# Optimization experiments

Hardware: AMD Instinct MI355X
Metric: run time of the kernel (lower is better)

The kernel has to match this reference:

```python
import jax, jax.numpy as jnp
import numpy as np

D_ENC, D_PRED, D_JOINT, VOCAB = 512, 512, 640, 1024


def setup_inputs() -> dict:
    key = jax.random.key(0)
    k1, k2, k3, k4, k5, k6 = jax.random.split(key, 6)
    B, T, U1 = 8, 256, 64
    enc_out = jax.random.normal(k1, (B, T, D_ENC), dtype=jnp.float32)
    pred_out = jax.random.normal(k2, (B, U1, D_PRED), dtype=jnp.float32)
    # Linear weights, torch convention [out, in]; kaiming-uniform-ish scale
    W_enc = jax.random.normal(k3, (D_JOINT, D_ENC), dtype=jnp.float32) / np.sqrt(D_ENC)
    W_pred = jax.random.normal(k4, (D_JOINT, D_PRED), dtype=jnp.float32) / np.sqrt(D_PRED)
    W_out = jax.random.normal(k5, (VOCAB, D_JOINT), dtype=jnp.float32) / np.sqrt(D_JOINT)
    b_out = jax.random.normal(k6, (VOCAB,), dtype=jnp.float32) * 0.01
    return {"enc_out": enc_out, "pred_out": pred_out, "W_enc": W_enc,
            "W_pred": W_pred, "W_out": W_out, "b_out": b_out}


def reference(enc_out, pred_out, W_enc, W_pred, W_out, b_out):
    # f: [B, T, d_joint], g: [B, U+1, d_joint]
    f = jnp.einsum("btd,jd->btj", enc_out, W_enc)
    g = jnp.einsum("bud,jd->buj", pred_out, W_pred)
    # broadcast add -> [B, T, U+1, d_joint], tanh, project to vocab
    combined = jnp.tanh(f[:, :, None, :] + g[:, None, :, :])
    logits = jnp.einsum("btuj,vj->btuv", combined, W_out) + b_out
    return logits
```

## Files before the change

### kernel.cpp

```cpp
#include <hip/hip_runtime.h>


typedef _Float16 f16x8 __attribute__((ext_vector_type(8)));
typedef float    f32x4 __attribute__((ext_vector_type(4)));

__device__ __forceinline__ float fast_tanh(float x) {
    float e = __builtin_amdgcn_exp2f(x * 2.88539008177792681472f);
    return 1.0f - 2.0f * __builtin_amdgcn_rcpf(e + 1.0f);
}

__device__ __forceinline__ void gll16(const void* g, void* l) {
    __builtin_amdgcn_global_load_lds(
        (const __attribute__((address_space(1))) void*)g,
        (__attribute__((address_space(3))) void*)l, 16, 0, 0);
}

__global__ __launch_bounds__(256) void fg_kernel(
    const float* __restrict__ enc, const float* __restrict__ pred,
    const float* __restrict__ Wenc, const float* __restrict__ Wpred,
    float* __restrict__ fg)
{
    __shared__ float As[64][36];
    __shared__ float WsT[32][68];

    const int bid = blockIdx.x;
    const int mt = bid / 10;
    const int nt = bid % 10;
    const int m0 = mt * 64;
    const int n0 = nt * 64;

    const float* Aptr;
    const float* Wptr;
    if (m0 < 2048) { Aptr = enc  + (size_t)m0 * 512;          Wptr = Wenc; }
    else           { Aptr = pred + (size_t)(m0 - 2048) * 512; Wptr = Wpred; }

    const int t  = threadIdx.x;
    const int ty = t >> 4;
    const int tx = t & 15;
    const int lr = t >> 2;
    const int lc = (t & 3) * 8;
    const int lane6 = t & 63;
    const int w8    = (t >> 6) * 8;

    float acc[4][4];
#pragma unroll
    for (int i = 0; i < 4; ++i)
#pragma unroll
        for (int j = 0; j < 4; ++j) acc[i][j] = 0.0f;

    for (int k0 = 0; k0 < 512; k0 += 32) {
        __syncthreads();
        {
            const float* sa = Aptr + (size_t)lr * 512 + k0 + lc;
            f32x4 a0 = *(const f32x4*)(sa);
            f32x4 a1 = *(const f32x4*)(sa + 4);
            *(f32x4*)&As[lr][lc]     = a0;
            *(f32x4*)&As[lr][lc + 4] = a1;
            const float* sw = Wptr + (size_t)(n0 + lane6) * 512 + k0 + w8;
            f32x4 w0 = *(const f32x4*)(sw);
            f32x4 w1 = *(const f32x4*)(sw + 4);
#pragma unroll
            for (int j = 0; j < 4; ++j) {
                WsT[w8 + j][lane6]     = w0[j];
                WsT[w8 + 4 + j][lane6] = w1[j];
            }
        }
        __syncthreads();
#pragma unroll
        for (int kk = 0; kk < 32; ++kk) {
            float av[4], bv[4];
#pragma unroll
            for (int i = 0; i < 4; ++i) av[i] = As[ty * 4 + i][kk];
#pragma unroll
            for (int j = 0; j < 4; ++j) bv[j] = WsT[kk][tx * 4 + j];
#pragma unroll
            for (int i = 0; i < 4; ++i)
#pragma unroll
                for (int j = 0; j < 4; ++j)
                    acc[i][j] = fmaf(av[i], bv[j], acc[i][j]);
        }
    }

#pragma unroll
    for (int i = 0; i < 4; ++i) {
        f32x4 v = { acc[i][0], acc[i][1], acc[i][2], acc[i][3] };
        *(f32x4*)&fg[(size_t)(m0 + ty * 4 + i) * 640 + n0 + tx * 4] = v;
    }
}

__global__ __launch_bounds__(256) void wconv_kernel(
    const float* __restrict__ W, _Float16* __restrict__ Wh)
{
    const int idx = (blockIdx.x * 256 + threadIdx.x) * 8;
    f32x4 a = *(const f32x4*)(W + idx);
    f32x4 b = *(const f32x4*)(W + idx + 4);
    f16x8 h;
#pragma unroll
    for (int j = 0; j < 4; ++j) { h[j] = (_Float16)a[j]; h[4 + j] = (_Float16)b[j]; }
    *(f16x8*)(Wh + idx) = h;
}

__global__ __launch_bounds__(256, 2) void joint_kernel(
    const float* __restrict__ fg, const _Float16* __restrict__ Wh,
    const float* __restrict__ bias, float* __restrict__ out)
{
    __shared__ _Float16 Ash0[64 * 40];
    __shared__ _Float16 Ash1[64 * 40];
    __shared__ _Float16 Bsh0[512 * 32];
    __shared__ _Float16 Bsh1[512 * 32];

    const int bid = blockIdx.x;
    const int pp  = bid >> 1;
    const int mt  = (pp & 7) * 256 + (pp >> 3);
    const int nt  = bid & 1;
    const int m0  = mt << 6;
    const int n0  = nt << 9;

    const int t    = threadIdx.x;
    const int lane = t & 63;
    const int wid  = t >> 6;
    const int wn   = wid;
    const int lr   = lane & 15;
    const int lk   = lane >> 4;

    const int r  = t >> 2;
    const int q  = t & 3;
    const int m  = m0 + r;
    const float* grow = fg + (size_t)(2048 + ((m >> 14) << 6) + (m & 63)) * 640;
    const float* frow = fg + (size_t)(m >> 6) * 640;

    int aoff[4];
#pragma unroll
    for (int mf = 0; mf < 4; ++mf)
        aoff[mf] = (mf * 16 + lr) * 40 + lk * 8;
    int boff[8];
#pragma unroll
    for (int nf = 0; nf < 8; ++nf) {
        const int brow = wn * 128 + nf * 16 + lr;
        const int slot = lk ^ (brow & 3) ^ ((brow >> 2) & 3);
        boff[nf] = brow * 32 + slot * 8;
    }
    const int awoff = r * 40 + q * 8;

    const _Float16* gsrc[8];
    int gdst[8];
#pragma unroll
    for (int i = 0; i < 8; ++i) {
        const int seg  = wid * 8 + i;
        const int row  = (seg << 4) + (lane >> 2);
        const int c    = (lane & 3) ^ (row & 3) ^ ((row >> 2) & 3);
        gsrc[i] = Wh + (size_t)(n0 + row) * 640 + c * 8;
        gdst[i] = seg << 9;
    }

    f32x4 acc[4][8];
#pragma unroll
    for (int i = 0; i < 4; ++i)
#pragma unroll
        for (int j = 0; j < 8; ++j) acc[i][j] = (f32x4){0.f, 0.f, 0.f, 0.f};

    {
#pragma unroll
        for (int i = 0; i < 8; ++i)
            gll16(gsrc[i], &Bsh0[gdst[i]]);
        f32x4 fv0 = *(const f32x4*)(frow + q * 8);
        f32x4 fv1 = *(const f32x4*)(frow + q * 8 + 4);
        f32x4 gv0 = *(const f32x4*)(grow + q * 8);
        f32x4 gv1 = *(const f32x4*)(grow + q * 8 + 4);
        f16x8 h;
#pragma unroll
        for (int j = 0; j < 4; ++j) {
            h[j]     = (_Float16)fast_tanh(fv0[j] + gv0[j]);
            h[4 + j] = (_Float16)fast_tanh(fv1[j] + gv1[j]);
        }
        *(f16x8*)&Ash0[awoff] = h;
        __syncthreads();
    }

#define JITER_FULL(K0, CA, CB, NA, NB)                                         \
    {                                                                          \
        const int kn_ = (K0) + 32;                                             \
        _Pragma("unroll")                                                      \
        for (int i = 0; i < 8; ++i)                                            \
            gll16(gsrc[i] + kn_, &NB[gdst[i]]);                                \
        f32x4 fv0_ = *(const f32x4*)(frow + kn_ + q * 8);                      \
        f32x4 fv1_ = *(const f32x4*)(frow + kn_ + q * 8 + 4);                  \
        f32x4 gv0_ = *(const f32x4*)(grow + kn_ + q * 8);                      \
        f32x4 gv1_ = *(const f32x4*)(grow + kn_ + q * 8 + 4);                  \
        f16x8 af[4], bf[8];                                                    \
        _Pragma("unroll")                                                      \
        for (int mf = 0; mf < 4; ++mf)                                         \
            af[mf] = *(const f16x8*)&CA[aoff[mf]];                             \
        _Pragma("unroll")                                                      \
        for (int nf = 0; nf < 8; ++nf)                                         \
            bf[nf] = *(const f16x8*)&CB[boff[nf]];                             \
        f16x8 h_;                                                              \
        _Pragma("unroll")                                                      \
        for (int j = 0; j < 4; ++j) {                                          \
            h_[j]     = (_Float16)fast_tanh(fv0_[j] + gv0_[j]);                \
            h_[4 + j] = (_Float16)fast_tanh(fv1_[j] + gv1_[j]);                \
        }                                                                      \
        _Pragma("unroll")                                                      \
        for (int mf = 0; mf < 4; ++mf)                                         \
            _Pragma("unroll")                                                  \
            for (int nf = 0; nf < 8; ++nf)                                     \
                acc[mf][nf] = __builtin_amdgcn_mfma_f32_16x16x32_f16(          \
                    af[mf], bf[nf], acc[mf][nf], 0, 0, 0);                     \
        *(f16x8*)&NA[awoff] = h_;                                              \
        __syncthreads();                                                       \
    }

#define JITER_LAST(CA, CB)                                                     \
    {                                                                          \
        f16x8 af[4], bf[8];                                                    \
        _Pragma("unroll")                                                      \
        for (int mf = 0; mf < 4; ++mf)                                         \
            af[mf] = *(const f16x8*)&CA[aoff[mf]];                             \
        _Pragma("unroll")                                                      \
        for (int nf = 0; nf < 8; ++nf)                                         \
            bf[nf] = *(const f16x8*)&CB[boff[nf]];                             \
        _Pragma("unroll")                                                      \
        for (int mf = 0; mf < 4; ++mf)                                         \
            _Pragma("unroll")                                                  \
            for (int nf = 0; nf < 8; ++nf)                                     \
                acc[mf][nf] = __builtin_amdgcn_mfma_f32_16x16x32_f16(          \
                    af[mf], bf[nf], acc[mf][nf], 0, 0, 0);                     \
    }

    for (int kc = 0; kc < 18; kc += 2) {
        JITER_FULL(kc * 32,      Ash0, Bsh0, Ash1, Bsh1);
        JITER_FULL(kc * 32 + 32, Ash1, Bsh1, Ash0, Bsh0);
    }
    JITER_FULL(576, Ash0, Bsh0, Ash1, Bsh1);
    JITER_LAST(Ash1, Bsh1);

#undef JITER_FULL
#undef JITER_LAST

    float bv[8];
#pragma unroll
    for (int nf = 0; nf < 8; ++nf)
        bv[nf] = bias[n0 + wn * 128 + nf * 16 + lr];

#pragma unroll
    for (int mf = 0; mf < 4; ++mf) {
#pragma unroll
        for (int rr = 0; rr < 4; ++rr) {
            const int row = m0 + mf * 16 + lk * 4 + rr;
            float* orow = out + (size_t)row * 1024 + n0 + wn * 128;
#pragma unroll
            for (int nf = 0; nf < 8; ++nf)
                orow[nf * 16 + lr] = acc[mf][nf][rr] + bv[nf];
        }
    }
}

extern "C" void kernel_launch(void* const* d_in, const int* in_sizes, int n_in,
                              void* d_out, int out_size, void* d_ws, size_t ws_size,
                              hipStream_t stream) {
    const float* enc   = (const float*)d_in[0];
    const float* pred  = (const float*)d_in[1];
    const float* Wenc  = (const float*)d_in[2];
    const float* Wpred = (const float*)d_in[3];
    const float* Wout  = (const float*)d_in[4];
    const float* bout  = (const float*)d_in[5];

    float*     fg = (float*)d_ws;
    _Float16*  Wh = (_Float16*)((char*)d_ws + 2560 * 640 * 4);

    fg_kernel<<<400, 256, 0, stream>>>(enc, pred, Wenc, Wpred, fg);
    wconv_kernel<<<320, 256, 0, stream>>>(Wout, Wh);
    joint_kernel<<<4096, 256, 0, stream>>>(fg, Wh, bout, (float*)d_out);
}
```

Before: 355.9 us.

## Split joint GEMM k-step into four MFMA phases interleaved with loads and tanh

```diff
diff --git a/kernel.cpp b/kernel.cpp
--- a/kernel.cpp
+++ b/kernel.cpp
@@ -177,54 +177,80 @@
         __syncthreads();
     }
 
+    f16x8 af[4];
+    f16x8 hstage;
+
+#define JP_MFMA(P, BF0, BF1)                                                   \
+        __builtin_amdgcn_s_barrier();                                          \
+        __builtin_amdgcn_sched_barrier(0);                                     \
+        __builtin_amdgcn_s_setprio(1);                                         \
+        _Pragma("unroll")                                                      \
+        for (int mf = 0; mf < 4; ++mf) {                                       \
+            acc[mf][2 * (P)]     = __builtin_amdgcn_mfma_f32_16x16x32_f16(     \
+                af[mf], BF0, acc[mf][2 * (P)], 0, 0, 0);                       \
+            acc[mf][2 * (P) + 1] = __builtin_amdgcn_mfma_f32_16x16x32_f16(     \
+                af[mf], BF1, acc[mf][2 * (P) + 1], 0, 0, 0);                   \
+        }                                                                      \
+        __builtin_amdgcn_s_setprio(0);                                         \
+        __builtin_amdgcn_s_barrier();
+
 #define JITER_FULL(K0, CA, CB, NA, NB)                                         \
     {                                                                          \
         const int kn_ = (K0) + 32;                                             \
-        _Pragma("unroll")                                                      \
-        for (int i = 0; i < 8; ++i)                                            \
-            gll16(gsrc[i] + kn_, &NB[gdst[i]]);                                \
+                                \
+        f16x8 bf0, bf1;                                                        \
+        _Pragma("unroll")                                                      \
+        for (int mf = 0; mf < 4; ++mf)                                         \
+            af[mf] = *(const f16x8*)&CA[aoff[mf]];                             \
+        bf0 = *(const f16x8*)&CB[boff[0]];                                     \
+        bf1 = *(const f16x8*)&CB[boff[1]];                                     \
         f32x4 fv0_ = *(const f32x4*)(frow + kn_ + q * 8);                      \
         f32x4 fv1_ = *(const f32x4*)(frow + kn_ + q * 8 + 4);                  \
         f32x4 gv0_ = *(const f32x4*)(grow + kn_ + q * 8);                      \
         f32x4 gv1_ = *(const f32x4*)(grow + kn_ + q * 8 + 4);                  \
-        f16x8 af[4], bf[8];                                                    \
+        _Pragma("unroll")                                                      \
+        for (int i = 0; i < 4; ++i)                                            \
+            gll16(gsrc[i] + kn_, &NB[gdst[i]]);                                \
+        JP_MFMA(0, bf0, bf1)                                                   \
+                                \
+        bf0 = *(const f16x8*)&CB[boff[2]];                                     \
+        bf1 = *(const f16x8*)&CB[boff[3]];                                     \
+        _Pragma("unroll")                                                      \
+        for (int i = 4; i < 8; ++i)                                            \
+            gll16(gsrc[i] + kn_, &NB[gdst[i]]);                                \
+        JP_MFMA(1, bf0, bf1)                                                   \
+                                \
+        bf0 = *(const f16x8*)&CB[boff[4]];                                     \
+        bf1 = *(const f16x8*)&CB[boff[5]];                                     \
+        _Pragma("unroll")                                                      \
+        for (int j = 0; j < 4; ++j) {                                          \
+            hstage[j]     = (_Float16)fast_tanh(fv0_[j] + gv0_[j]);            \
+            hstage[4 + j] = (_Float16)fast_tanh(fv1_[j] + gv1_[j]);            \
+        }                                                                      \
+        JP_MFMA(2, bf0, bf1)                                                   \
+                                \
+        bf0 = *(const f16x8*)&CB[boff[6]];                                     \
+        bf1 = *(const f16x8*)&CB[boff[7]];                                     \
+        *(f16x8*)&NA[awoff] = hstage;                                          \
+        JP_MFMA(3, bf0, bf1)                                                   \
+        __syncthreads();                                                       \
+    }
+
+#define JITER_LAST(CA, CB)                                                     \
+    {                                                                          \
+        f16x8 bf[8];                                                           \
         _Pragma("unroll")                                                      \
         for (int mf = 0; mf < 4; ++mf)                                         \
             af[mf] = *(const f16x8*)&CA[aoff[mf]];                             \
         _Pragma("unroll")                                                      \
         for (int nf = 0; nf < 8; ++nf)                                         \
             bf[nf] = *(const f16x8*)&CB[boff[nf]];                             \
-        f16x8 h_;                                                              \
-        _Pragma("unroll")                                                      \
-        for (int j = 0; j < 4; ++j) {                                          \
-            h_[j]     = (_Float16)fast_tanh(fv0_[j] + gv0_[j]);                \
-            h_[4 + j] = (_Float16)fast_tanh(fv1_[j] + gv1_[j]);                \
-        }                                                                      \
         _Pragma("unroll")                                                      \
         for (int mf = 0; mf < 4; ++mf)                                         \
             _Pragma("unroll")                                                  \
             for (int nf = 0; nf < 8; ++nf)                                     \
                 acc[mf][nf] = __builtin_amdgcn_mfma_f32_16x16x32_f16(          \
                     af[mf], bf[nf], acc[mf][nf], 0, 0, 0);                     \
-        *(f16x8*)&NA[awoff] = h_;                                              \
-        __syncthreads();                                                       \
-    }
-
-#define JITER_LAST(CA, CB)                                                     \
-    {                                                                          \
-        f16x8 af[4], bf[8];                                                    \
-        _Pragma("unroll")                                                      \
-        for (int mf = 0; mf < 4; ++mf)                                         \
-            af[mf] = *(const f16x8*)&CA[aoff[mf]];                             \
-        _Pragma("unroll")                                                      \
-        for (int nf = 0; nf < 8; ++nf)                                         \
-            bf[nf] = *(const f16x8*)&CB[boff[nf]];                             \
-        _Pragma("unroll")                                                      \
-        for (int mf = 0; mf < 4; ++mf)                                         \
-            _Pragma("unroll")                                                  \
-            for (int nf = 0; nf < 8; ++nf)                                     \
-                acc[mf][nf] = __builtin_amdgcn_mfma_f32_16x16x32_f16(          \
-                    af[mf], bf[nf], acc[mf][nf], 0, 0, 0);                     \
     }
 
     for (int kc = 0; kc < 18; kc += 2) {
@@ -236,6 +262,7 @@
 
 #undef JITER_FULL
 #undef JITER_LAST
+#undef JP_MFMA
 
     float bv[8];
 #pragma unroll
```

Result: no change. 351.5 us (-1.3%).
